# Optimization experiments

Measured on AMD Instinct MI355X. Metric: run time of the kernel, lower is better.

## Reference

```python
import jax, jax.numpy as jnp
import numpy as np

B, S, D, H = 2, 2048, 2048, 16
HD = D // H  # 128


def setup_inputs() -> dict:
    key = jax.random.key(0)
    ks = jax.random.split(key, 5)
    x = jax.random.normal(ks[0], (B, S, D), dtype=jnp.float32)
    scale = 1.0 / np.sqrt(D)
    wq = jax.random.normal(ks[1], (D, D), dtype=jnp.float32) * scale
    wk = jax.random.normal(ks[2], (D, D), dtype=jnp.float32) * scale
    wv = jax.random.normal(ks[3], (D, D), dtype=jnp.float32) * scale
    wo = jax.random.normal(ks[4], (D, D), dtype=jnp.float32) * scale
    # RoPE frequencies: theta = 10000, freqs_cis[t, j] = exp(i * t / theta^(2j/HD))
    inv_freq = 1.0 / (10000.0 ** (jnp.arange(0, HD, 2, dtype=jnp.float32) / HD))  # [HD/2]
    t = jnp.arange(S, dtype=jnp.float32)
    ang = jnp.outer(t, inv_freq)  # [S, HD/2]
    freqs_cos = jnp.cos(ang)
    freqs_sin = jnp.sin(ang)
    # Additive causal mask [S, S]
    neg = jnp.float32(-1e9)
    mask = jnp.triu(jnp.full((S, S), neg, dtype=jnp.float32), k=1)
    return {"x": x, "wq": wq, "wk": wk, "wv": wv, "wo": wo,
            "freqs_cos": freqs_cos, "freqs_sin": freqs_sin,
            "mask": mask, "start_pos": 0}


def _rope(t, cos, sin):
    # t: [B, S, H, HD]; cos/sin: [S, HD/2] broadcast as [1, S, 1, HD/2]
    tr = t.reshape(t.shape[:-1] + (HD // 2, 2))
    xr, xi = tr[..., 0], tr[..., 1]
    c = cos[None, :, None, :]
    s = sin[None, :, None, :]
    out_r = xr * c - xi * s
    out_i = xr * s + xi * c
    return jnp.stack([out_r, out_i], axis=-1).reshape(t.shape)


def reference(x, wq, wk, wv, wo, freqs_cos, freqs_sin, mask, start_pos):
    bsz, seqlen, _ = x.shape
    # nn.Linear: y = x @ W.T
    xq = jnp.einsum('bsd,ed->bse', x, wq).reshape(bsz, seqlen, H, HD)
    xk = jnp.einsum('bsd,ed->bse', x, wk).reshape(bsz, seqlen, H, HD)
    xv = jnp.einsum('bsd,ed->bse', x, wv).reshape(bsz, seqlen, H, HD)
    xq = _rope(xq, freqs_cos, freqs_sin)
    xk = _rope(xk, freqs_cos, freqs_sin)
    # [B, H, S, HD]
    xq = xq.transpose(0, 2, 1, 3)
    xk = xk.transpose(0, 2, 1, 3)
    xv = xv.transpose(0, 2, 1, 3)
    scores = jnp.einsum('bhqd,bhkd->bhqk', xq, xk) / jnp.sqrt(jnp.float32(HD))
    scores = scores + mask[None, None, :, :]
    probs = jax.nn.softmax(scores.astype(jnp.float32), axis=-1).astype(xq.dtype)
    out = jnp.einsum('bhqk,bhkd->bhqd', probs, xv)
    out = out.transpose(0, 2, 1, 3).reshape(bsz, seqlen, H * HD)
    return jnp.einsum('bse,de->bsd', out, wo)
```

## Files before the change

### kernel.cpp

```cpp
#include <hip/hip_runtime.h>


#define SQ 2048
#define DQ 2048
#define HQ 16
#define HDQ 128

typedef short bf16x8 __attribute__((ext_vector_type(8)));
typedef float f32x4 __attribute__((ext_vector_type(4)));

#define WAITVM8 asm volatile("s_waitcnt vmcnt(8)" ::: "memory")
#define WAITVM0 asm volatile("s_waitcnt vmcnt(0)" ::: "memory")

__device__ __forceinline__ short f2bf(float f) {
  union { float f; unsigned u; } v; v.f = f;
  unsigned r = (v.u + 0x7FFFu + ((v.u >> 16) & 1u)) >> 16;
  return (short)r;
}
__device__ __forceinline__ float bf2f(short b) {
  union { unsigned u; float f; } v; v.u = ((unsigned)(unsigned short)b) << 16;
  return v.f;
}
__device__ __forceinline__ void gload_lds16(const void* g, void* l) {
  __builtin_amdgcn_global_load_lds(
      (const __attribute__((address_space(1))) void*)g,
      (__attribute__((address_space(3))) void*)l, 16, 0, 0);
}

__global__ void cvt_kernel(const float* __restrict__ in, short* __restrict__ out, int nvec) {
  int i = blockIdx.x * blockDim.x + threadIdx.x;
  if (i >= nvec) return;
  const f32x4* p = (const f32x4*)in + (size_t)i * 2;
  f32x4 a = p[0], b = p[1];
  bf16x8 o;
  o[0] = f2bf(a[0]); o[1] = f2bf(a[1]); o[2] = f2bf(a[2]); o[3] = f2bf(a[3]);
  o[4] = f2bf(b[0]); o[5] = f2bf(b[1]); o[6] = f2bf(b[2]); o[7] = f2bf(b[3]);
  *((bf16x8*)out + i) = o;
}

__global__ void rope_kernel(short* __restrict__ t, const float* __restrict__ cosT,
                            const float* __restrict__ sinT, float scale, int nvec) {
  int i = blockIdx.x * blockDim.x + threadIdx.x;
  if (i >= nvec) return;
  size_t off = (size_t)i * 8;
  int hd0 = (int)(off & 127);
  int s = (int)((off >> 7) & 2047);
  bf16x8 v = *((const bf16x8*)(t + off));
  f32x4 c  = *(const f32x4*)(cosT + (size_t)s * 64 + (hd0 >> 1));
  f32x4 sn = *(const f32x4*)(sinT + (size_t)s * 64 + (hd0 >> 1));
  bf16x8 o;
#pragma unroll
  for (int p = 0; p < 4; ++p) {
    float xr = bf2f(v[2 * p]), xi = bf2f(v[2 * p + 1]);
    o[2 * p]     = f2bf((xr * c[p] - xi * sn[p]) * scale);
    o[2 * p + 1] = f2bf((xr * sn[p] + xi * c[p]) * scale);
  }
  *((bf16x8*)(t + off)) = o;
}

__global__ void vtrans_kernel(const short* __restrict__ vb, short* __restrict__ vtb) {
  __shared__ __align__(16) short tile[64][72];
  int bh = blockIdx.z, s0 = blockIdx.y * 64, d0 = blockIdx.x * 64;
  int tid = threadIdx.x;
#pragma unroll
  for (int it = 0; it < 2; ++it) {
    int vi = it * 256 + tid;
    int r = vi >> 3, c8 = (vi & 7) * 8;
    bf16x8 v = *(const bf16x8*)&vb[((size_t)bh * SQ + s0 + r) * HDQ + d0 + c8];
    *(bf16x8*)&tile[r][c8] = v;
  }
  __syncthreads();
#pragma unroll
  for (int it = 0; it < 2; ++it) {
    int vi = it * 256 + tid;
    int d = vi >> 3, s8 = (vi & 7) * 8;
    bf16x8 o;
#pragma unroll
    for (int j = 0; j < 8; ++j) o[j] = tile[s8 + j][d];
    *(bf16x8*)&vtb[((size_t)bh * HDQ + d0 + d) * SQ + s0 + s8] = o;
  }
}

template <int MODE>
__global__ __launch_bounds__(256, 2) void gemm_bt(const short* __restrict__ A,
                                                  const short* __restrict__ W,
                                                  short* __restrict__ oQ, short* __restrict__ oK,
                                                  short* __restrict__ oV, float* __restrict__ oF) {
  const int K = DQ;
  __shared__ __align__(16) short As[128 * 32];
  __shared__ __align__(16) short Bs[128 * 32];
  int n0 = blockIdx.x * 128, m0 = blockIdx.y * 128;
  const short* Bw = (MODE == 0) ? (W + (size_t)blockIdx.z * DQ * DQ) : W;
  int tid = threadIdx.x, w = tid >> 6, lane = tid & 63;
  int wr = w >> 1, wc = w & 1;
  int ar = lane >> 2, acol = (lane & 3) * 8;
  f32x4 acc[4][4] = {};
  int lra = wr * 64 + (lane & 15), lrb = wc * 64 + (lane & 15), kc = (lane >> 4) * 8;
  for (int k0 = 0; k0 < K; k0 += 32) {
    __syncthreads();
#pragma unroll
    for (int i = 0; i < 2; ++i) {
      int c = w * 2 + i;
      int r = c * 16 + ar;
      gload_lds16(A + (size_t)(m0 + r) * K + k0 + acol, &As[c * 512]);
      gload_lds16(Bw + (size_t)(n0 + r) * K + k0 + acol, &Bs[c * 512]);
    }
    __syncthreads();
    bf16x8 af[4], bfr[4];
#pragma unroll
    for (int f = 0; f < 4; ++f) {
      af[f] = *(const bf16x8*)&As[(lra + f * 16) * 32 + kc];
      bfr[f] = *(const bf16x8*)&Bs[(lrb + f * 16) * 32 + kc];
    }
#pragma unroll
    for (int mf = 0; mf < 4; ++mf)
#pragma unroll
      for (int nf = 0; nf < 4; ++nf)
        acc[mf][nf] = __builtin_amdgcn_mfma_f32_16x16x32_bf16(af[mf], bfr[nf], acc[mf][nf], 0, 0, 0);
  }
  short* oT = nullptr;
  if (MODE == 0) oT = (blockIdx.z == 0) ? oQ : (blockIdx.z == 1) ? oK : oV;
#pragma unroll
  for (int mf = 0; mf < 4; ++mf) {
    int mb = m0 + wr * 64 + mf * 16 + (lane >> 4) * 4;
#pragma unroll
    for (int nf = 0; nf < 4; ++nf) {
      int n = n0 + wc * 64 + nf * 16 + (lane & 15);
#pragma unroll
      for (int j = 0; j < 4; ++j) {
        int m = mb + j;
        float v = acc[mf][nf][j];
        if (MODE == 0) {
          int b = m >> 11, s = m & 2047, h = n >> 7, hd = n & 127;
          oT[(((size_t)(b * HQ + h)) * SQ + s) * HDQ + hd] = f2bf(v);
        } else {
          oF[(size_t)m * DQ + n] = v;
        }
      }
    }
  }
}

__device__ __forceinline__ void stage_kv(const short* kbase, const short* vbase, int k0,
                                         short* KsB, short* VtB, int w, int lane) {
#pragma unroll
  for (int i = 0; i < 4; ++i) {
    int c = w * 4 + i;
    int r = c * 4 + (lane >> 4);
    int col = (lane & 15) * 8;
    gload_lds16(kbase + (size_t)(k0 + r) * HDQ + (col ^ ((r & 7) << 3)), KsB + c * 512);
    int d = c * 8 + (lane >> 3);
    int jj = (lane & 7) * 8;
    gload_lds16(vbase + (size_t)d * SQ + k0 + (jj ^ ((d & 7) << 3)), VtB + c * 512);
  }
}

__global__ __launch_bounds__(256, 1) void flash_kernel(const short* __restrict__ qb,
                                                       const short* __restrict__ kb,
                                                       const short* __restrict__ vtb,
                                                       short* __restrict__ ab) {
  __shared__ __align__(16) short Ks[2][64 * 128];
  __shared__ __align__(16) short Vt[2][128 * 64];
  __shared__ __align__(16) short Pl[4][32 * 72];
  int x = blockIdx.x, bh = blockIdx.y;
  int tid = threadIdx.x, w = tid >> 6, lane = tid & 63;
  const short* qbase = qb + (size_t)bh * SQ * HDQ;
  const short* kbase = kb + (size_t)bh * SQ * HDQ;
  const short* vbase = vtb + (size_t)bh * HDQ * SQ;
  int b = bh >> 4, h = bh & 15;

#pragma unroll 1
  for (int pass = 0; pass < 2; ++pass) {
    int qt = pass ? (15 - x) : x;
    int q0 = qt * 128;
    bf16x8 qf[2][4];
    {
      int qr = q0 + w * 32 + (lane & 15);
      int kq = (lane >> 4) * 8;
#pragma unroll
      for (int i = 0; i < 2; ++i)
#pragma unroll
        for (int c = 0; c < 4; ++c)
          qf[i][c] = *(const bf16x8*)&qbase[(size_t)(qr + i * 16) * HDQ + c * 32 + kq];
    }
    f32x4 oacc[2][8] = {};
    f32x4 m_st[2], l_st[2];
#pragma unroll
    for (int i = 0; i < 2; ++i) {
      m_st[i] = f32x4{-1e30f, -1e30f, -1e30f, -1e30f};
      l_st[i] = f32x4{0.f, 0.f, 0.f, 0.f};
    }
    int nt = 2 * qt + 2;
    stage_kv(kbase, vbase, 0, Ks[0], Vt[0], w, lane);
#pragma unroll 1
    for (int t = 0; t < nt; ++t) {
      int cur = t & 1;
      int k0 = t * 64;
      __builtin_amdgcn_s_barrier();
      if (t + 1 < nt) {
        stage_kv(kbase, vbase, (t + 1) * 64, Ks[cur ^ 1], Vt[cur ^ 1], w, lane);
        WAITVM8;
      } else {
        WAITVM0;
      }
      __builtin_amdgcn_s_barrier();
      f32x4 sacc[2][4] = {};
      __builtin_amdgcn_s_setprio(1);
#pragma unroll
      for (int nf = 0; nf < 4; ++nf) {
        int rk = nf * 16 + (lane & 15);
#pragma unroll
        for (int cc = 0; cc < 4; ++cc) {
          int ck = cc * 32 + (lane >> 4) * 8;
          bf16x8 kf = *(const bf16x8*)&Ks[cur][rk * 128 + (ck ^ ((rk & 7) << 3))];
          sacc[0][nf] = __builtin_amdgcn_mfma_f32_16x16x32_bf16(qf[0][cc], kf, sacc[0][nf], 0, 0, 0);
          sacc[1][nf] = __builtin_amdgcn_mfma_f32_16x16x32_bf16(qf[1][cc], kf, sacc[1][nf], 0, 0, 0);
        }
      }
      __builtin_amdgcn_s_setprio(0);
      if (k0 + 63 > q0) {
#pragma unroll
        for (int i = 0; i < 2; ++i)
#pragma unroll
          for (int nf = 0; nf < 4; ++nf)
#pragma unroll
            for (int j = 0; j < 4; ++j) {
              int q = q0 + w * 32 + i * 16 + (lane >> 4) * 4 + j;
              int k = k0 + nf * 16 + (lane & 15);
              if (k > q) sacc[i][nf][j] -= 1e9f;
            }
      }
#pragma unroll
      for (int i = 0; i < 2; ++i) {
        f32x4 mt = sacc[i][0];
#pragma unroll
        for (int nf = 1; nf < 4; ++nf)
#pragma unroll
          for (int j = 0; j < 4; ++j) mt[j] = fmaxf(mt[j], sacc[i][nf][j]);
#pragma unroll
        for (int d = 1; d < 16; d <<= 1)
#pragma unroll
          for (int j = 0; j < 4; ++j) mt[j] = fmaxf(mt[j], __shfl_xor(mt[j], d));
        f32x4 mn, al;
#pragma unroll
        for (int j = 0; j < 4; ++j) {
          mn[j] = fmaxf(m_st[i][j], mt[j]);
          al[j] = exp2f(m_st[i][j] - mn[j]);
        }
#pragma unroll
        for (int df = 0; df < 8; ++df) oacc[i][df] *= al;
        f32x4 rs = {0.f, 0.f, 0.f, 0.f};
#pragma unroll
        for (int nf = 0; nf < 4; ++nf)
#pragma unroll
          for (int j = 0; j < 4; ++j) {
            float p = exp2f(sacc[i][nf][j] - mn[j]);
            rs[j] += p;
            Pl[w][(i * 16 + (lane >> 4) * 4 + j) * 72 + nf * 16 + (lane & 15)] = f2bf(p);
          }
        l_st[i] = l_st[i] * al + rs;
        m_st[i] = mn;
      }
      __builtin_amdgcn_s_setprio(1);
#pragma unroll
      for (int cc = 0; cc < 2; ++cc) {
        bf16x8 pf0 = *(const bf16x8*)&Pl[w][((lane & 15)) * 72 + cc * 32 + (lane >> 4) * 8];
        bf16x8 pf1 = *(const bf16x8*)&Pl[w][(16 + (lane & 15)) * 72 + cc * 32 + (lane >> 4) * 8];
#pragma unroll
        for (int df = 0; df < 8; ++df) {
          int rd = df * 16 + (lane & 15);
          int cv = cc * 32 + (lane >> 4) * 8;
          bf16x8 vf = *(const bf16x8*)&Vt[cur][rd * 64 + (cv ^ ((rd & 7) << 3))];
          oacc[0][df] = __builtin_amdgcn_mfma_f32_16x16x32_bf16(pf0, vf, oacc[0][df], 0, 0, 0);
          oacc[1][df] = __builtin_amdgcn_mfma_f32_16x16x32_bf16(pf1, vf, oacc[1][df], 0, 0, 0);
        }
      }
      __builtin_amdgcn_s_setprio(0);
    }
#pragma unroll
    for (int i = 0; i < 2; ++i) {
#pragma unroll
      for (int d = 1; d < 16; d <<= 1)
#pragma unroll
        for (int j = 0; j < 4; ++j) l_st[i][j] += __shfl_xor(l_st[i][j], d);
      f32x4 inv;
#pragma unroll
      for (int j = 0; j < 4; ++j) inv[j] = 1.0f / l_st[i][j];
#pragma unroll
      for (int df = 0; df < 8; ++df)
#pragma unroll
        for (int j = 0; j < 4; ++j) {
          int q = q0 + w * 32 + i * 16 + (lane >> 4) * 4 + j;
          int dd = df * 16 + (lane & 15);
          ab[((size_t)b * SQ + q) * DQ + h * HDQ + dd] = f2bf(oacc[i][df][j] * inv[j]);
        }
    }
  }
}

extern "C" void kernel_launch(void* const* d_in, const int* in_sizes, int n_in,
                              void* d_out, int out_size, void* d_ws, size_t ws_size,
                              hipStream_t stream) {
  (void)in_sizes; (void)n_in; (void)out_size; (void)ws_size;
  const float* x  = (const float*)d_in[0];
  const float* wq = (const float*)d_in[1];
  const float* wk = (const float*)d_in[2];
  const float* wv = (const float*)d_in[3];
  const float* wo = (const float*)d_in[4];
  const float* fc = (const float*)d_in[5];
  const float* fs = (const float*)d_in[6];
  float* out = (float*)d_out;

  short* xb  = (short*)d_ws;
  short* wqb = xb + (size_t)8388608;
  short* wkb = wqb + (size_t)4194304;
  short* wvb = wkb + (size_t)4194304;
  short* wob = wvb + (size_t)4194304;
  short* qb  = wob + (size_t)4194304;
  short* kb  = qb + (size_t)8388608;
  short* ab  = kb + (size_t)8388608;
  short* vb  = (short*)d_out;
  short* vtb = vb + (size_t)8388608;

  cvt_kernel<<<4096, 256, 0, stream>>>(x, xb, 1048576);
  cvt_kernel<<<2048, 256, 0, stream>>>(wq, wqb, 524288);
  cvt_kernel<<<2048, 256, 0, stream>>>(wk, wkb, 524288);
  cvt_kernel<<<2048, 256, 0, stream>>>(wv, wvb, 524288);
  cvt_kernel<<<2048, 256, 0, stream>>>(wo, wob, 524288);

  gemm_bt<0><<<dim3(16, 32, 3), 256, 0, stream>>>(xb, wqb, qb, kb, vb, nullptr);

  rope_kernel<<<4096, 256, 0, stream>>>(qb, fc, fs, 0.12751744779976827f, 1048576);
  rope_kernel<<<4096, 256, 0, stream>>>(kb, fc, fs, 1.0f, 1048576);

  vtrans_kernel<<<dim3(2, 32, 32), 256, 0, stream>>>(vb, vtb);

  flash_kernel<<<dim3(8, 32), 256, 0, stream>>>(qb, kb, vtb, ab);

  gemm_bt<1><<<dim3(16, 32, 1), 256, 0, stream>>>(ab, wob, nullptr, nullptr, nullptr, out);
}
```

Before: 331.3 us.

## Shrink flash query tile to 64 rows and launch more blocks

Flash attention now gives each block a single 64-row query tile (16 rows per wave) instead of two paired 128-row passes. The grid grows from 8x32 to 32x32 blocks, with the tile order reversed for half the heads to balance causal work. Launch bounds now allow two blocks per CU, and the P staging buffer and register state shrink to match. This raises occupancy and spreads the causal load more evenly across the CUs. The cost is that each K/V tile is reused across fewer query rows, so K/V global traffic per block rises.

```diff
diff --git a/kernel.cpp b/kernel.cpp
--- a/kernel.cpp
+++ b/kernel.cpp
@@ -155,147 +155,125 @@
   }
 }
 
-__global__ __launch_bounds__(256, 1) void flash_kernel(const short* __restrict__ qb,
+__global__ __launch_bounds__(256, 2) void flash_kernel(const short* __restrict__ qb,
                                                        const short* __restrict__ kb,
                                                        const short* __restrict__ vtb,
                                                        short* __restrict__ ab) {
   __shared__ __align__(16) short Ks[2][64 * 128];
   __shared__ __align__(16) short Vt[2][128 * 64];
-  __shared__ __align__(16) short Pl[4][32 * 72];
+  __shared__ __align__(16) short Pl[4][16 * 68];
   int x = blockIdx.x, bh = blockIdx.y;
+  int qt = (bh & 8) ? (31 - x) : x;
+  int q0 = qt * 64;
   int tid = threadIdx.x, w = tid >> 6, lane = tid & 63;
   const short* qbase = qb + (size_t)bh * SQ * HDQ;
   const short* kbase = kb + (size_t)bh * SQ * HDQ;
   const short* vbase = vtb + (size_t)bh * HDQ * SQ;
   int b = bh >> 4, h = bh & 15;
 
+  bf16x8 qf[4];
+  {
+    int qr = q0 + w * 16 + (lane & 15);
+    int kq = (lane >> 4) * 8;
+#pragma unroll
+    for (int c = 0; c < 4; ++c)
+      qf[c] = *(const bf16x8*)&qbase[(size_t)qr * HDQ + c * 32 + kq];
+  }
+  f32x4 oacc[8] = {};
+  f32x4 m_st = f32x4{-1e30f, -1e30f, -1e30f, -1e30f};
+  f32x4 l_st = f32x4{0.f, 0.f, 0.f, 0.f};
+  int nt = qt + 1;
+  stage_kv(kbase, vbase, 0, Ks[0], Vt[0], w, lane);
 #pragma unroll 1
-  for (int pass = 0; pass < 2; ++pass) {
-    int qt = pass ? (15 - x) : x;
-    int q0 = qt * 128;
-    bf16x8 qf[2][4];
-    {
-      int qr = q0 + w * 32 + (lane & 15);
-      int kq = (lane >> 4) * 8;
-#pragma unroll
-      for (int i = 0; i < 2; ++i)
-#pragma unroll
-        for (int c = 0; c < 4; ++c)
-          qf[i][c] = *(const bf16x8*)&qbase[(size_t)(qr + i * 16) * HDQ + c * 32 + kq];
-    }
-    f32x4 oacc[2][8] = {};
-    f32x4 m_st[2], l_st[2];
-#pragma unroll
-    for (int i = 0; i < 2; ++i) {
-      m_st[i] = f32x4{-1e30f, -1e30f, -1e30f, -1e30f};
-      l_st[i] = f32x4{0.f, 0.f, 0.f, 0.f};
-    }
-    int nt = 2 * qt + 2;
-    stage_kv(kbase, vbase, 0, Ks[0], Vt[0], w, lane);
-#pragma unroll 1
-    for (int t = 0; t < nt; ++t) {
-      int cur = t & 1;
-      int k0 = t * 64;
-      __builtin_amdgcn_s_barrier();
-      if (t + 1 < nt) {
-        stage_kv(kbase, vbase, (t + 1) * 64, Ks[cur ^ 1], Vt[cur ^ 1], w, lane);
-        WAITVM8;
-      } else {
-        WAITVM0;
+  for (int t = 0; t < nt; ++t) {
+    int cur = t & 1;
+    int k0 = t * 64;
+    __builtin_amdgcn_s_barrier();
+    if (t + 1 < nt) {
+      stage_kv(kbase, vbase, (t + 1) * 64, Ks[cur ^ 1], Vt[cur ^ 1], w, lane);
+      WAITVM8;
+    } else {
+      WAITVM0;
+    }
+    __builtin_amdgcn_s_barrier();
+    f32x4 sacc[4] = {};
+    __builtin_amdgcn_s_setprio(1);
+#pragma unroll
+    for (int nf = 0; nf < 4; ++nf) {
+      int rk = nf * 16 + (lane & 15);
+#pragma unroll
+      for (int cc = 0; cc < 4; ++cc) {
+        int ck = cc * 32 + (lane >> 4) * 8;
+        bf16x8 kf = *(const bf16x8*)&Ks[cur][rk * 128 + (ck ^ ((rk & 7) << 3))];
+        sacc[nf] = __builtin_amdgcn_mfma_f32_16x16x32_bf16(qf[cc], kf, sacc[nf], 0, 0, 0);
       }
-      __builtin_amdgcn_s_barrier();
-      f32x4 sacc[2][4] = {};
-      __builtin_amdgcn_s_setprio(1);
-#pragma unroll
-      for (int nf = 0; nf < 4; ++nf) {
-        int rk = nf * 16 + (lane & 15);
-#pragma unroll
-        for (int cc = 0; cc < 4; ++cc) {
-          int ck = cc * 32 + (lane >> 4) * 8;
-          bf16x8 kf = *(const bf16x8*)&Ks[cur][rk * 128 + (ck ^ ((rk & 7) << 3))];
-          sacc[0][nf] = __builtin_amdgcn_mfma_f32_16x16x32_bf16(qf[0][cc], kf, sacc[0][nf], 0, 0, 0);
-          sacc[1][nf] = __builtin_amdgcn_mfma_f32_16x16x32_bf16(qf[1][cc], kf, sacc[1][nf], 0, 0, 0);
+    }
+    __builtin_amdgcn_s_setprio(0);
+    if (t == nt - 1) {
+#pragma unroll
+      for (int nf = 0; nf < 4; ++nf)
+#pragma unroll
+        for (int j = 0; j < 4; ++j) {
+          int q = q0 + w * 16 + (lane >> 4) * 4 + j;
+          int k = k0 + nf * 16 + (lane & 15);
+          if (k > q) sacc[nf][j] -= 1e9f;
         }
+    }
+    f32x4 mt = sacc[0];
+#pragma unroll
+    for (int nf = 1; nf < 4; ++nf)
+#pragma unroll
+      for (int j = 0; j < 4; ++j) mt[j] = fmaxf(mt[j], sacc[nf][j]);
+#pragma unroll
+    for (int d = 1; d < 16; d <<= 1)
+#pragma unroll
+      for (int j = 0; j < 4; ++j) mt[j] = fmaxf(mt[j], __shfl_xor(mt[j], d));
+    f32x4 mn, al;
+#pragma unroll
+    for (int j = 0; j < 4; ++j) {
+      mn[j] = fmaxf(m_st[j], mt[j]);
+      al[j] = exp2f(m_st[j] - mn[j]);
+    }
+#pragma unroll
+    for (int df = 0; df < 8; ++df) oacc[df] *= al;
+#pragma unroll
+    for (int nf = 0; nf < 4; ++nf)
+#pragma unroll
+      for (int j = 0; j < 4; ++j) {
+        float p = exp2f(sacc[nf][j] - mn[j]);
+        l_st[j] = l_st[j] * ((nf == 0) ? al[j] : 1.0f) + p;
+        Pl[w][((lane >> 4) * 4 + j) * 68 + nf * 16 + (lane & 15)] = f2bf(p);
       }
-      __builtin_amdgcn_s_setprio(0);
-      if (k0 + 63 > q0) {
-#pragma unroll
-        for (int i = 0; i < 2; ++i)
-#pragma unroll
-          for (int nf = 0; nf < 4; ++nf)
-#pragma unroll
-            for (int j = 0; j < 4; ++j) {
-              int q = q0 + w * 32 + i * 16 + (lane >> 4) * 4 + j;
-              int k = k0 + nf * 16 + (lane & 15);
-              if (k > q) sacc[i][nf][j] -= 1e9f;
-            }
+    m_st = mn;
+    __builtin_amdgcn_s_setprio(1);
+#pragma unroll
+    for (int cc = 0; cc < 2; ++cc) {
+      bf16x8 pf = *(const bf16x8*)&Pl[w][(lane & 15) * 68 + cc * 32 + (lane >> 4) * 8];
+#pragma unroll
+      for (int df = 0; df < 8; ++df) {
+        int rd = df * 16 + (lane & 15);
+        int cv = cc * 32 + (lane >> 4) * 8;
+        bf16x8 vf = *(const bf16x8*)&Vt[cur][rd * 64 + (cv ^ ((rd & 7) << 3))];
+        oacc[df] = __builtin_amdgcn_mfma_f32_16x16x32_bf16(pf, vf, oacc[df], 0, 0, 0);
       }
-#pragma unroll
-      for (int i = 0; i < 2; ++i) {
-        f32x4 mt = sacc[i][0];
-#pragma unroll
-        for (int nf = 1; nf < 4; ++nf)
-#pragma unroll
-          for (int j = 0; j < 4; ++j) mt[j] = fmaxf(mt[j], sacc[i][nf][j]);
-#pragma unroll
-        for (int d = 1; d < 16; d <<= 1)
-#pragma unroll
-          for (int j = 0; j < 4; ++j) mt[j] = fmaxf(mt[j], __shfl_xor(mt[j], d));
-        f32x4 mn, al;
-#pragma unroll
-        for (int j = 0; j < 4; ++j) {
-          mn[j] = fmaxf(m_st[i][j], mt[j]);
-          al[j] = exp2f(m_st[i][j] - mn[j]);
-        }
-#pragma unroll
-        for (int df = 0; df < 8; ++df) oacc[i][df] *= al;
-        f32x4 rs = {0.f, 0.f, 0.f, 0.f};
-#pragma unroll
-        for (int nf = 0; nf < 4; ++nf)
-#pragma unroll
-          for (int j = 0; j < 4; ++j) {
-            float p = exp2f(sacc[i][nf][j] - mn[j]);
-            rs[j] += p;
-            Pl[w][(i * 16 + (lane >> 4) * 4 + j) * 72 + nf * 16 + (lane & 15)] = f2bf(p);
-          }
-        l_st[i] = l_st[i] * al + rs;
-        m_st[i] = mn;
-      }
-      __builtin_amdgcn_s_setprio(1);
-#pragma unroll
-      for (int cc = 0; cc < 2; ++cc) {
-        bf16x8 pf0 = *(const bf16x8*)&Pl[w][((lane & 15)) * 72 + cc * 32 + (lane >> 4) * 8];
-        bf16x8 pf1 = *(const bf16x8*)&Pl[w][(16 + (lane & 15)) * 72 + cc * 32 + (lane >> 4) * 8];
-#pragma unroll
-        for (int df = 0; df < 8; ++df) {
-          int rd = df * 16 + (lane & 15);
-          int cv = cc * 32 + (lane >> 4) * 8;
-          bf16x8 vf = *(const bf16x8*)&Vt[cur][rd * 64 + (cv ^ ((rd & 7) << 3))];
-          oacc[0][df] = __builtin_amdgcn_mfma_f32_16x16x32_bf16(pf0, vf, oacc[0][df], 0, 0, 0);
-          oacc[1][df] = __builtin_amdgcn_mfma_f32_16x16x32_bf16(pf1, vf, oacc[1][df], 0, 0, 0);
-        }
-      }
-      __builtin_amdgcn_s_setprio(0);
-    }
-#pragma unroll
-    for (int i = 0; i < 2; ++i) {
-#pragma unroll
-      for (int d = 1; d < 16; d <<= 1)
-#pragma unroll
-        for (int j = 0; j < 4; ++j) l_st[i][j] += __shfl_xor(l_st[i][j], d);
-      f32x4 inv;
-#pragma unroll
-      for (int j = 0; j < 4; ++j) inv[j] = 1.0f / l_st[i][j];
-#pragma unroll
-      for (int df = 0; df < 8; ++df)
-#pragma unroll
-        for (int j = 0; j < 4; ++j) {
-          int q = q0 + w * 32 + i * 16 + (lane >> 4) * 4 + j;
-          int dd = df * 16 + (lane & 15);
-          ab[((size_t)b * SQ + q) * DQ + h * HDQ + dd] = f2bf(oacc[i][df][j] * inv[j]);
-        }
-    }
-  }
+    }
+    __builtin_amdgcn_s_setprio(0);
+  }
+#pragma unroll
+  for (int d = 1; d < 16; d <<= 1)
+#pragma unroll
+    for (int j = 0; j < 4; ++j) l_st[j] += __shfl_xor(l_st[j], d);
+  f32x4 inv;
+#pragma unroll
+  for (int j = 0; j < 4; ++j) inv[j] = 1.0f / l_st[j];
+#pragma unroll
+  for (int df = 0; df < 8; ++df)
+#pragma unroll
+    for (int j = 0; j < 4; ++j) {
+      int q = q0 + w * 16 + (lane >> 4) * 4 + j;
+      int dd = df * 16 + (lane & 15);
+      ab[((size_t)b * SQ + q) * DQ + h * HDQ + dd] = f2bf(oacc[df][j] * inv[j]);
+    }
 }
 
 extern "C" void kernel_launch(void* const* d_in, const int* in_sizes, int n_in,
@@ -335,7 +313,7 @@
 
   vtrans_kernel<<<dim3(2, 32, 32), 256, 0, stream>>>(vb, vtb);
 
-  flash_kernel<<<dim3(8, 32), 256, 0, stream>>>(qb, kb, vtb, ab);
+  flash_kernel<<<dim3(32, 32), 256, 0, stream>>>(qb, kb, vtb, ab);
 
   gemm_bt<1><<<dim3(16, 32, 1), 256, 0, stream>>>(ab, wob, nullptr, nullptr, nullptr, out);
 }
```

Result: no change. 334.3 us (+0.9%).
